# Performance work log

Hardware: AMD Instinct MI355X
Metric: run time of the kernel (lower is better)

The kernel has to match this reference:

```python
import jax, jax.numpy as jnp
import numpy as np

D_MODEL = 1024
D_CODEX = 64
CODEX_SIZE = 8192
BETA = 1.0
EPS_NORM = 1e-12
EPS_LN = 1e-5


def l2norm(x):
    # F.normalize(p=2, dim=-1, eps=1e-12): x / max(||x||, eps)
    n = jnp.sqrt(jnp.sum(x * x, axis=-1, keepdims=True))
    return x / jnp.maximum(n, EPS_NORM)


def setup_inputs() -> dict:
    key = jax.random.key(0)
    ks = jax.random.split(key, 8)
    B, S = 4, 2048
    Z = jax.random.normal(ks[0], (B, S, D_MODEL), dtype=jnp.float32)
    W1 = 0.02 * jax.random.normal(ks[1], (D_MODEL, D_MODEL), dtype=jnp.float32)
    b1 = jnp.zeros((D_MODEL,), dtype=jnp.float32)
    W2 = 0.02 * jax.random.normal(ks[2], (D_MODEL, D_CODEX), dtype=jnp.float32)
    b2 = jnp.zeros((D_CODEX,), dtype=jnp.float32)
    codex = l2norm(jax.random.normal(ks[3], (CODEX_SIZE, D_CODEX), dtype=jnp.float32))
    ln_w = jnp.ones((D_CODEX,), dtype=jnp.float32)
    ln_b = jnp.zeros((D_CODEX,), dtype=jnp.float32)
    Wp = 0.02 * jax.random.normal(ks[4], (D_CODEX, D_MODEL), dtype=jnp.float32)
    bp = jnp.zeros((D_MODEL,), dtype=jnp.float32)
    return {"Z": Z, "W1": W1, "b1": b1, "W2": W2, "b2": b2,
            "codex": codex, "ln_w": ln_w, "ln_b": ln_b, "Wp": Wp, "bp": bp}


def reference(Z, W1, b1, W2, b2, codex, ln_w, ln_b, Wp, bp):
    # pre_proj: Linear -> Tanh -> Linear, then l2-normalize into codex space
    Z_e = jnp.tanh(Z @ W1 + b1) @ W2 + b2            # (B, S, d_codex)
    Z_e = l2norm(Z_e)
    flat = Z_e.reshape(-1, D_CODEX)                  # (N, d_codex)
    # squared-L2 distances: |z|^2 + |c|^2 - 2 z.c
    dists = (jnp.sum(flat * flat, axis=-1, keepdims=True)
             + jnp.sum(codex * codex, axis=-1)[None, :]
             - 2.0 * jnp.einsum('nd,cd->nc', flat, codex))  # (N, K)
    idxs = jnp.argmin(dists, axis=-1).reshape(Z_e.shape[:-1])  # (B, S)
    codex_probs = jax.nn.one_hot(idxs, CODEX_SIZE, dtype=Z_e.dtype)  # (B, S, K)
    Z_q = codex[idxs]                                 # (B, S, d_codex)
    # commitment loss (codex is an EMA buffer, no gradient through it)
    loss = BETA * jnp.mean((jax.lax.stop_gradient(Z_q) - Z_e) ** 2)
    # straight-through estimator
    Z_q = Z_e + jax.lax.stop_gradient(Z_q - Z_e)
    # layernorm over d_codex
    mu = jnp.mean(Z_q, axis=-1, keepdims=True)
    var = jnp.mean((Z_q - mu) ** 2, axis=-1, keepdims=True)
    Z_q = (Z_q - mu) * jax.lax.rsqrt(var + EPS_LN) * ln_w + ln_b
    # post_proj back to d_model
    Z_q = Z_q @ Wp + bp                               # (B, S, d_model)
    return Z_q, loss, codex_probs
```

## Files before the change

kernel.cpp:

```cpp
#include <hip/hip_runtime.h>
#include <math.h>
#include <stdint.h>

#define N_TOK   8192
#define DMODEL  1024
#define DCODEX  64
#define KCODES  8192

typedef short short8 __attribute__((ext_vector_type(8)));
typedef float f32x16 __attribute__((ext_vector_type(16)));

union Frag { short8 s; uint2 u[2]; };

__device__ __forceinline__ unsigned short f2bf(float f) {
    unsigned u = __float_as_uint(f);
    unsigned r = u + 0x7FFFu + ((u >> 16) & 1u);
    return (unsigned short)(r >> 16);
}
__device__ __forceinline__ float bf2f(unsigned short h) {
    return __uint_as_float(((unsigned)h) << 16);
}

__global__ __launch_bounds__(256) void codenorm_kernel(const float* __restrict__ codex,
                                                       float* __restrict__ cn2) {
    int k = blockIdx.x * 256 + threadIdx.x;
    const float4* p = (const float4*)(codex + (size_t)k * DCODEX);
    float s = 0.f;
#pragma unroll
    for (int i = 0; i < 16; ++i) {
        float4 v = p[i];
        s += v.x * v.x + v.y * v.y + v.z * v.z + v.w * v.w;
    }
    cn2[k] = s;
}

__global__ __launch_bounds__(256) void split_w1_kernel(const float* __restrict__ W1,
                                                       unsigned short* __restrict__ t0,
                                                       unsigned short* __restrict__ t1,
                                                       unsigned short* __restrict__ t2) {
    __shared__ float tile[32][33];
    const int tid = threadIdx.x;
    const int k0 = blockIdx.x * 32;
    const int n0 = blockIdx.y * 32;
    {
        int i = tid >> 3, j4 = (tid & 7) * 4;
        float4 v = *(const float4*)(W1 + (size_t)(k0 + i) * DMODEL + n0 + j4);
        tile[i][j4 + 0] = v.x; tile[i][j4 + 1] = v.y;
        tile[i][j4 + 2] = v.z; tile[i][j4 + 3] = v.w;
    }
    __syncthreads();
    int n = tid >> 3, kq = (tid & 7) * 4;
    ushort4 h0, h1, h2;
#pragma unroll
    for (int c = 0; c < 4; ++c) {
        float f = tile[kq + c][n];
        unsigned short a0 = f2bf(f);
        float r1 = f - bf2f(a0);
        unsigned short a1 = f2bf(r1);
        float r2 = r1 - bf2f(a1);
        unsigned short a2 = f2bf(r2);
        ((unsigned short*)&h0)[c] = a0;
        ((unsigned short*)&h1)[c] = a1;
        ((unsigned short*)&h2)[c] = a2;
    }
    size_t off = (size_t)(n0 + n) * DMODEL + k0 + kq;
    *(ushort4*)(t0 + off) = h0;
    *(ushort4*)(t1 + off) = h1;
    *(ushort4*)(t2 + off) = h2;
}

__global__ __launch_bounds__(256) void gemm1_mfma_kernel(const float* __restrict__ Z,
                                                         const unsigned short* __restrict__ W1t0,
                                                         const unsigned short* __restrict__ W1t1,
                                                         const unsigned short* __restrict__ W1t2,
                                                         const float* __restrict__ b1,
                                                         float* __restrict__ H) {
    __shared__ unsigned short Ash[3][128][36];
    __shared__ unsigned short Bsh[3][128][36];
    const int tid = threadIdx.x;
    const int row0 = blockIdx.x * 128;
    const int col0 = blockIdx.y * 128;
    const int wave = tid >> 6;
    const int lane = tid & 63;
    const int lrow = lane & 31;
    const int lhalf = lane >> 5;
    const int wm = wave >> 1, wn = wave & 1;

    f32x16 acc[2][2];
#pragma unroll
    for (int i = 0; i < 2; ++i)
#pragma unroll
        for (int j = 0; j < 2; ++j)
#pragma unroll
            for (int r = 0; r < 16; ++r) acc[i][j][r] = 0.f;

    for (int k0 = 0; k0 < DMODEL; k0 += 32) {
        __syncthreads();
#pragma unroll
        for (int t = 0; t < 4; ++t) {
            int q = tid + t * 256;
            int r = q >> 3, kc = (q & 7) * 4;
            float4 v = *(const float4*)(Z + (size_t)(row0 + r) * DMODEL + k0 + kc);
            float f[4] = {v.x, v.y, v.z, v.w};
            unsigned h0[4], h1[4], h2[4];
#pragma unroll
            for (int c = 0; c < 4; ++c) {
                unsigned short a0 = f2bf(f[c]);
                float r1 = f[c] - bf2f(a0);
                unsigned short a1 = f2bf(r1);
                float r2 = r1 - bf2f(a1);
                unsigned short a2 = f2bf(r2);
                h0[c] = a0; h1[c] = a1; h2[c] = a2;
            }
            uint2 p0 = make_uint2(h0[0] | (h0[1] << 16), h0[2] | (h0[3] << 16));
            uint2 p1 = make_uint2(h1[0] | (h1[1] << 16), h1[2] | (h1[3] << 16));
            uint2 p2 = make_uint2(h2[0] | (h2[1] << 16), h2[2] | (h2[3] << 16));
            *(uint2*)&Ash[0][r][kc] = p0;
            *(uint2*)&Ash[1][r][kc] = p1;
            *(uint2*)&Ash[2][r][kc] = p2;
        }
#pragma unroll
        for (int t = 0; t < 6; ++t) {
            int e = tid + t * 256;
            int l = e >> 9;
            int rem = e & 511;
            int n = rem >> 2, kq = (rem & 3) * 8;
            const unsigned short* src = (l == 0) ? W1t0 : (l == 1) ? W1t1 : W1t2;
            uint4 v = *(const uint4*)(src + (size_t)(col0 + n) * DMODEL + k0 + kq);
            *(uint2*)&Bsh[l][n][kq]     = make_uint2(v.x, v.y);
            *(uint2*)&Bsh[l][n][kq + 4] = make_uint2(v.z, v.w);
        }
        __syncthreads();
#pragma unroll
        for (int mk = 0; mk < 2; ++mk) {
            const int kb = mk * 16 + lhalf * 8;
            Frag ah[2], am[2], al[2], bh[2], bm[2], bl[2];
#pragma unroll
            for (int ti = 0; ti < 2; ++ti) {
                int rA = wm * 64 + ti * 32 + lrow;
                ah[ti].u[0] = *(const uint2*)&Ash[0][rA][kb];
                ah[ti].u[1] = *(const uint2*)&Ash[0][rA][kb + 4];
                am[ti].u[0] = *(const uint2*)&Ash[1][rA][kb];
                am[ti].u[1] = *(const uint2*)&Ash[1][rA][kb + 4];
                al[ti].u[0] = *(const uint2*)&Ash[2][rA][kb];
                al[ti].u[1] = *(const uint2*)&Ash[2][rA][kb + 4];
            }
#pragma unroll
            for (int tj = 0; tj < 2; ++tj) {
                int rB = wn * 64 + tj * 32 + lrow;
                bh[tj].u[0] = *(const uint2*)&Bsh[0][rB][kb];
                bh[tj].u[1] = *(const uint2*)&Bsh[0][rB][kb + 4];
                bm[tj].u[0] = *(const uint2*)&Bsh[1][rB][kb];
                bm[tj].u[1] = *(const uint2*)&Bsh[1][rB][kb + 4];
                bl[tj].u[0] = *(const uint2*)&Bsh[2][rB][kb];
                bl[tj].u[1] = *(const uint2*)&Bsh[2][rB][kb + 4];
            }
#pragma unroll
            for (int ti = 0; ti < 2; ++ti)
#pragma unroll
                for (int tj = 0; tj < 2; ++tj) {
                    acc[ti][tj] = __builtin_amdgcn_mfma_f32_32x32x16_bf16(ah[ti].s, bh[tj].s, acc[ti][tj], 0, 0, 0);
                    acc[ti][tj] = __builtin_amdgcn_mfma_f32_32x32x16_bf16(ah[ti].s, bm[tj].s, acc[ti][tj], 0, 0, 0);
                    acc[ti][tj] = __builtin_amdgcn_mfma_f32_32x32x16_bf16(am[ti].s, bh[tj].s, acc[ti][tj], 0, 0, 0);
                    acc[ti][tj] = __builtin_amdgcn_mfma_f32_32x32x16_bf16(am[ti].s, bm[tj].s, acc[ti][tj], 0, 0, 0);
                    acc[ti][tj] = __builtin_amdgcn_mfma_f32_32x32x16_bf16(ah[ti].s, bl[tj].s, acc[ti][tj], 0, 0, 0);
                    acc[ti][tj] = __builtin_amdgcn_mfma_f32_32x32x16_bf16(al[ti].s, bh[tj].s, acc[ti][tj], 0, 0, 0);
                }
        }
    }

    float b1v[2];
#pragma unroll
    for (int tj = 0; tj < 2; ++tj) b1v[tj] = b1[col0 + wn * 64 + tj * 32 + lrow];
#pragma unroll
    for (int ti = 0; ti < 2; ++ti)
#pragma unroll
        for (int tj = 0; tj < 2; ++tj) {
            int col = col0 + wn * 64 + tj * 32 + lrow;
#pragma unroll
            for (int r = 0; r < 16; ++r) {
                int row = row0 + wm * 64 + ti * 32 + (r & 3) + 8 * (r >> 2) + 4 * lhalf;
                H[(size_t)row * DMODEL + col] = tanhf(acc[ti][tj][r] + b1v[tj]);
            }
        }
}

__global__ __launch_bounds__(256) void gemm2_norm_kernel(const float* __restrict__ H,
                                                         const float* __restrict__ W2,
                                                         const float* __restrict__ b2,
                                                         float* __restrict__ Ze) {
    __shared__ float As[64][36];
    __shared__ float Bs[64][68];
    const int tid = threadIdx.x;
    const int row0 = blockIdx.x * 32;
    const int ty = tid >> 4, tx = tid & 15;

    float acc[2][4];
#pragma unroll
    for (int i = 0; i < 2; ++i)
#pragma unroll
        for (int j = 0; j < 4; ++j) acc[i][j] = 0.f;

    for (int k0 = 0; k0 < DMODEL; k0 += 64) {
        __syncthreads();
#pragma unroll
        for (int t = 0; t < 2; ++t) {
            int q = tid + t * 256;
            int r = q >> 4, k4 = (q & 15) * 4;
            float4 v = *(const float4*)(H + (size_t)(row0 + r) * DMODEL + k0 + k4);
            As[k4 + 0][r] = v.x; As[k4 + 1][r] = v.y;
            As[k4 + 2][r] = v.z; As[k4 + 3][r] = v.w;
        }
#pragma unroll
        for (int t = 0; t < 4; ++t) {
            int q = tid + t * 256;
            int kk = q >> 4, c4 = (q & 15) * 4;
            *(float4*)&Bs[kk][c4] = *(const float4*)(W2 + (size_t)(k0 + kk) * DCODEX + c4);
        }
        __syncthreads();
#pragma unroll
        for (int k = 0; k < 64; ++k) {
            float2 a = *(const float2*)&As[k][ty * 2];
            float4 b = *(const float4*)&Bs[k][tx * 4];
            float bw[4] = {b.x, b.y, b.z, b.w};
#pragma unroll
            for (int j = 0; j < 4; ++j) {
                acc[0][j] = fmaf(a.x, bw[j], acc[0][j]);
                acc[1][j] = fmaf(a.y, bw[j], acc[1][j]);
            }
        }
    }
    float4 b2v4 = *(const float4*)(b2 + tx * 4);
    float b2v[4] = {b2v4.x, b2v4.y, b2v4.z, b2v4.w};
#pragma unroll
    for (int i = 0; i < 2; ++i) {
        float e[4];
#pragma unroll
        for (int j = 0; j < 4; ++j) e[j] = acc[i][j] + b2v[j];
        float ss = e[0] * e[0] + e[1] * e[1] + e[2] * e[2] + e[3] * e[3];
        ss += __shfl_xor(ss, 8, 64);
        ss += __shfl_xor(ss, 4, 64);
        ss += __shfl_xor(ss, 2, 64);
        ss += __shfl_xor(ss, 1, 64);
        float nrm = fmaxf(sqrtf(ss), 1e-12f);
        float o[4];
#pragma unroll
        for (int j = 0; j < 4; ++j) o[j] = e[j] / nrm;
        *(float4*)(Ze + (size_t)(row0 + ty * 2 + i) * DCODEX + tx * 4) = *(float4*)&o[0];
    }
}

__device__ __forceinline__ unsigned fenc(float f) {
    unsigned u = __float_as_uint(f);
    return (u & 0x80000000u) ? ~u : (u | 0x80000000u);
}

__global__ __launch_bounds__(256) void dist_argmin_kernel(const float* __restrict__ Ze,
                                                          const float* __restrict__ codex,
                                                          const float* __restrict__ cn2,
                                                          unsigned long long* __restrict__ gbest) {
    __shared__ float Zs[64][132];
    __shared__ float Cs[32][132];
    __shared__ unsigned long long red[128];
    const int tid = threadIdx.x;
    const int row0 = blockIdx.x * 128;
    const int strip0 = blockIdx.y * 1024;
    const int ty = tid >> 4, tx = tid & 15;

    if (tid < 128) red[tid] = 0xFFFFFFFFFFFFFFFFull;
#pragma unroll
    for (int t = 0; t < 8; ++t) {
        int q = tid + t * 256;
        int r = q >> 4, d4 = (q & 15) * 4;
        float4 v = *(const float4*)(Ze + (size_t)(row0 + r) * DCODEX + d4);
        Zs[d4 + 0][r] = v.x; Zs[d4 + 1][r] = v.y;
        Zs[d4 + 2][r] = v.z; Zs[d4 + 3][r] = v.w;
    }

    float bv[8];
    int bi[8];
#pragma unroll
    for (int i = 0; i < 8; ++i) { bv[i] = INFINITY; bi[i] = 0; }

    for (int c0 = 0; c0 < 1024; c0 += 128) {
        const int cbase = strip0 + c0;
        float cn[8];
        *(float4*)&cn[0] = *(const float4*)(cn2 + cbase + tx * 4);
        *(float4*)&cn[4] = *(const float4*)(cn2 + cbase + 64 + tx * 4);
        float s[8][8];
#pragma unroll
        for (int i = 0; i < 8; ++i)
#pragma unroll
            for (int j = 0; j < 8; ++j) s[i][j] = 0.f;

        for (int h = 0; h < 2; ++h) {
            __syncthreads();
#pragma unroll
            for (int t = 0; t < 4; ++t) {
                int q = tid + t * 256;
                int c = q >> 3, d4 = (q & 7) * 4;
                float4 v = *(const float4*)(codex + (size_t)(cbase + c) * DCODEX + h * 32 + d4);
                Cs[d4 + 0][c] = v.x; Cs[d4 + 1][c] = v.y;
                Cs[d4 + 2][c] = v.z; Cs[d4 + 3][c] = v.w;
            }
            __syncthreads();
#pragma unroll
            for (int d = 0; d < 32; ++d) {
                float a[8], b[8];
                *(float4*)&a[0] = *(const float4*)&Zs[h * 32 + d][ty * 4];
                *(float4*)&a[4] = *(const float4*)&Zs[h * 32 + d][64 + ty * 4];
                *(float4*)&b[0] = *(const float4*)&Cs[d][tx * 4];
                *(float4*)&b[4] = *(const float4*)&Cs[d][64 + tx * 4];
#pragma unroll
                for (int i = 0; i < 8; ++i)
#pragma unroll
                    for (int j = 0; j < 8; ++j)
                        s[i][j] = fmaf(a[i], b[j], s[i][j]);
            }
        }
#pragma unroll
        for (int i = 0; i < 8; ++i)
#pragma unroll
            for (int j = 0; j < 8; ++j) {
                float dist = fmaf(-2.0f, s[i][j], cn[j]);
                int col = cbase + ((j < 4) ? (tx * 4 + j) : (64 + tx * 4 + j - 4));
                if (dist < bv[i]) { bv[i] = dist; bi[i] = col; }
            }
    }
#pragma unroll
    for (int i = 0; i < 8; ++i) {
        int li = (i < 4) ? (ty * 4 + i) : (64 + ty * 4 + i - 4);
        unsigned long long key =
            ((unsigned long long)fenc(bv[i]) << 32) | (unsigned)bi[i];
        atomicMin(&red[li], key);
    }
    __syncthreads();
    if (tid < 128) atomicMin(&gbest[row0 + tid], red[tid]);
}

__global__ __launch_bounds__(256) void zero_scatter_kernel(const unsigned long long* __restrict__ gbest,
                                                           float* __restrict__ probs) {
    size_t g = (size_t)blockIdx.x * 256 + threadIdx.x;
    int row = (int)(g >> 11);
    int c4i = (int)(g & 2047);
    unsigned id = (unsigned)(gbest[row] & 0xFFFFFFFFull);
    float4 v = {0.f, 0.f, 0.f, 0.f};
    if ((id >> 2) == (unsigned)c4i) ((float*)&v)[id & 3] = 1.0f;
    *(float4*)(probs + ((size_t)row << 13) + ((size_t)c4i << 2)) = v;
}

__global__ __launch_bounds__(256) void ln_loss_kernel(const unsigned long long* __restrict__ gbest,
                                                      const float* __restrict__ codex,
                                                      const float* __restrict__ Ze,
                                                      const float* __restrict__ ln_w,
                                                      const float* __restrict__ ln_b,
                                                      float* __restrict__ Aln,
                                                      float* __restrict__ loss) {
    const int tid = threadIdx.x;
    const int w = tid >> 6, l = tid & 63;
    const int row = blockIdx.x * 4 + w;
    int id = (int)(unsigned)(gbest[row] & 0xFFFFFFFFull);
    float zq = codex[(size_t)id * DCODEX + l];
    float ze = Ze[(size_t)row * DCODEX + l];
    float dlt = zq - ze;
    float val = ze + dlt;
    float s = val;
#pragma unroll
    for (int m = 32; m >= 1; m >>= 1) s += __shfl_xor(s, m, 64);
    float mu = s * 0.015625f;
    float c = val - mu;
    float v2 = c * c;
#pragma unroll
    for (int m = 32; m >= 1; m >>= 1) v2 += __shfl_xor(v2, m, 64);
    float var = v2 * 0.015625f;
    float y = c * (1.0f / sqrtf(var + 1e-5f)) * ln_w[l] + ln_b[l];
    Aln[(size_t)row * DCODEX + l] = y;
    float d2 = dlt * dlt;
#pragma unroll
    for (int m = 32; m >= 1; m >>= 1) d2 += __shfl_xor(d2, m, 64);
    if (l == 0) atomicAdd(loss, d2 * (1.0f / 524288.0f));
}

__global__ __launch_bounds__(256) void gemm3_kernel(const float* __restrict__ Aln,
                                                    const float* __restrict__ Wp,
                                                    const float* __restrict__ bp,
                                                    float* __restrict__ Zq) {
    __shared__ float As[64][132];
    __shared__ float Bs[64][68];
    const int tid = threadIdx.x;
    const int row0 = blockIdx.x * 128;
    const int col0 = blockIdx.y * 64;
    const int ty = tid >> 4, tx = tid & 15;

#pragma unroll
    for (int t = 0; t < 8; ++t) {
        int q = tid + t * 256;
        int r = q >> 4, d4 = (q & 15) * 4;
        float4 v = *(const float4*)(Aln + (size_t)(row0 + r) * DCODEX + d4);
        As[d4 + 0][r] = v.x; As[d4 + 1][r] = v.y;
        As[d4 + 2][r] = v.z; As[d4 + 3][r] = v.w;
    }
#pragma unroll
    for (int t = 0; t < 4; ++t) {
        int q = tid + t * 256;
        int kk = q >> 4, c4 = (q & 15) * 4;
        *(float4*)&Bs[kk][c4] = *(const float4*)(Wp + (size_t)kk * DMODEL + col0 + c4);
    }
    __syncthreads();

    float acc[8][4];
#pragma unroll
    for (int i = 0; i < 8; ++i)
#pragma unroll
        for (int j = 0; j < 4; ++j) acc[i][j] = 0.f;
#pragma unroll
    for (int k = 0; k < 64; ++k) {
        float a[8];
        *(float4*)&a[0] = *(const float4*)&As[k][ty * 4];
        *(float4*)&a[4] = *(const float4*)&As[k][64 + ty * 4];
        float4 b = *(const float4*)&Bs[k][tx * 4];
        float bw[4] = {b.x, b.y, b.z, b.w};
#pragma unroll
        for (int i = 0; i < 8; ++i)
#pragma unroll
            for (int j = 0; j < 4; ++j)
                acc[i][j] = fmaf(a[i], bw[j], acc[i][j]);
    }
    float4 bp4 = *(const float4*)(bp + col0 + tx * 4);
    float bb[4] = {bp4.x, bp4.y, bp4.z, bp4.w};
#pragma unroll
    for (int half = 0; half < 2; ++half)
#pragma unroll
        for (int i = 0; i < 4; ++i) {
            int r = row0 + half * 64 + ty * 4 + i;
            float o[4];
#pragma unroll
            for (int j = 0; j < 4; ++j) o[j] = acc[half * 4 + i][j] + bb[j];
            *(float4*)(Zq + (size_t)r * DMODEL + col0 + tx * 4) = *(float4*)&o[0];
        }
}

extern "C" void kernel_launch(void* const* d_in, const int* in_sizes, int n_in,
                              void* d_out, int out_size, void* d_ws, size_t ws_size,
                              hipStream_t stream) {
    const float* Z     = (const float*)d_in[0];
    const float* W1    = (const float*)d_in[1];
    const float* b1    = (const float*)d_in[2];
    const float* W2    = (const float*)d_in[3];
    const float* b2    = (const float*)d_in[4];
    const float* codex = (const float*)d_in[5];
    const float* ln_w  = (const float*)d_in[6];
    const float* ln_b  = (const float*)d_in[7];
    const float* Wp    = (const float*)d_in[8];
    const float* bp    = (const float*)d_in[9];

    float* out      = (float*)d_out;
    float* Zq_out   = out;
    float* loss_out = out + (size_t)N_TOK * DMODEL;
    float* probs    = loss_out + 1;

    char* ws = (char*)d_ws;
    float* H   = (float*)ws;
    float* Aln = H;
    float* Ze  = H + (size_t)N_TOK * DMODEL;
    float* cn2 = Ze + (size_t)N_TOK * DCODEX;
    unsigned long long* gbest = (unsigned long long*)(cn2 + KCODES);
    unsigned short* W1t0 = (unsigned short*)(gbest + N_TOK);
    unsigned short* W1t1 = W1t0 + (size_t)DMODEL * DMODEL;
    unsigned short* W1t2 = W1t1 + (size_t)DMODEL * DMODEL;

    hipMemsetAsync(loss_out, 0, sizeof(float), stream);
    hipMemsetAsync(gbest, 0xFF, (size_t)N_TOK * sizeof(unsigned long long), stream);

    codenorm_kernel<<<KCODES / 256, 256, 0, stream>>>(codex, cn2);
    split_w1_kernel<<<dim3(DMODEL / 32, DMODEL / 32), 256, 0, stream>>>(W1, W1t0, W1t1, W1t2);
    gemm1_mfma_kernel<<<dim3(N_TOK / 128, DMODEL / 128), 256, 0, stream>>>(Z, W1t0, W1t1, W1t2, b1, H);
    gemm2_norm_kernel<<<N_TOK / 32, 256, 0, stream>>>(H, W2, b2, Ze);
    dist_argmin_kernel<<<dim3(N_TOK / 128, KCODES / 1024), 256, 0, stream>>>(Ze, codex, cn2, gbest);
    zero_scatter_kernel<<<(int)(((size_t)N_TOK * KCODES / 4) / 256), 256, 0, stream>>>(gbest, probs);
    ln_loss_kernel<<<N_TOK / 4, 256, 0, stream>>>(gbest, codex, Ze, ln_w, ln_b, Aln, loss_out);
    gemm3_kernel<<<dim3(N_TOK / 128, DMODEL / 64), 256, 0, stream>>>(Aln, Wp, bp, Zq_out);
}
```

Baseline: 731.5 us.

## Move distance GEMM to split-bf16 MFMA and pre-split Z outside gemm1

Replaces the FP32 FMA distance/argmin kernel with an MFMA kernel that uses a three-way bf16 split (six products per tile) on pre-split Ze and codex arrays, reducing argmin with wave shuffles and a 64-bit atomicMin. It also pre-splits Z into three bf16 planes in a separate pass so gemm1 only loads bf16 tiles instead of splitting inside every block. The cost is extra split kernels, more workspace, extra global traffic for the Z planes, and more blocks doing atomics on gbest. Split-bf16 accuracy could also flip argmin ties in rare cases.

```diff
diff --git a/kernel.cpp b/kernel.cpp
--- a/kernel.cpp
+++ b/kernel.cpp
@@ -32,6 +32,30 @@
         s += v.x * v.x + v.y * v.y + v.z * v.z + v.w * v.w;
     }
     cn2[k] = s;
+}
+
+__global__ __launch_bounds__(256) void split3_kernel(const float* __restrict__ src,
+                                                     unsigned short* __restrict__ p0,
+                                                     unsigned short* __restrict__ p1,
+                                                     unsigned short* __restrict__ p2) {
+    size_t i4 = ((size_t)blockIdx.x * 256 + threadIdx.x) * 4;
+    float4 v = *(const float4*)(src + i4);
+    float f[4] = {v.x, v.y, v.z, v.w};
+    ushort4 h0, h1, h2;
+#pragma unroll
+    for (int c = 0; c < 4; ++c) {
+        unsigned short a0 = f2bf(f[c]);
+        float r1 = f[c] - bf2f(a0);
+        unsigned short a1 = f2bf(r1);
+        float r2 = r1 - bf2f(a1);
+        unsigned short a2 = f2bf(r2);
+        ((unsigned short*)&h0)[c] = a0;
+        ((unsigned short*)&h1)[c] = a1;
+        ((unsigned short*)&h2)[c] = a2;
+    }
+    *(ushort4*)(p0 + i4) = h0;
+    *(ushort4*)(p1 + i4) = h1;
+    *(ushort4*)(p2 + i4) = h2;
 }
 
 __global__ __launch_bounds__(256) void split_w1_kernel(const float* __restrict__ W1,
@@ -69,7 +93,9 @@
     *(ushort4*)(t2 + off) = h2;
 }
 
-__global__ __launch_bounds__(256) void gemm1_mfma_kernel(const float* __restrict__ Z,
+__global__ __launch_bounds__(256) void gemm1_mfma_kernel(const unsigned short* __restrict__ Zt0,
+                                                         const unsigned short* __restrict__ Zt1,
+                                                         const unsigned short* __restrict__ Zt2,
                                                          const unsigned short* __restrict__ W1t0,
                                                          const unsigned short* __restrict__ W1t1,
                                                          const unsigned short* __restrict__ W1t2,
@@ -86,6 +112,9 @@
     const int lhalf = lane >> 5;
     const int wm = wave >> 1, wn = wave & 1;
 
+    const unsigned short* Ap[3] = {Zt0, Zt1, Zt2};
+    const unsigned short* Bp[3] = {W1t0, W1t1, W1t2};
+
     f32x16 acc[2][2];
 #pragma unroll
     for (int i = 0; i < 2; ++i)
@@ -97,38 +126,18 @@
     for (int k0 = 0; k0 < DMODEL; k0 += 32) {
         __syncthreads();
 #pragma unroll
-        for (int t = 0; t < 4; ++t) {
-            int q = tid + t * 256;
-            int r = q >> 3, kc = (q & 7) * 4;
-            float4 v = *(const float4*)(Z + (size_t)(row0 + r) * DMODEL + k0 + kc);
-            float f[4] = {v.x, v.y, v.z, v.w};
-            unsigned h0[4], h1[4], h2[4];
-#pragma unroll
-            for (int c = 0; c < 4; ++c) {
-                unsigned short a0 = f2bf(f[c]);
-                float r1 = f[c] - bf2f(a0);
-                unsigned short a1 = f2bf(r1);
-                float r2 = r1 - bf2f(a1);
-                unsigned short a2 = f2bf(r2);
-                h0[c] = a0; h1[c] = a1; h2[c] = a2;
-            }
-            uint2 p0 = make_uint2(h0[0] | (h0[1] << 16), h0[2] | (h0[3] << 16));
-            uint2 p1 = make_uint2(h1[0] | (h1[1] << 16), h1[2] | (h1[3] << 16));
-            uint2 p2 = make_uint2(h2[0] | (h2[1] << 16), h2[2] | (h2[3] << 16));
-            *(uint2*)&Ash[0][r][kc] = p0;
-            *(uint2*)&Ash[1][r][kc] = p1;
-            *(uint2*)&Ash[2][r][kc] = p2;
-        }
-#pragma unroll
-        for (int t = 0; t < 6; ++t) {
-            int e = tid + t * 256;
-            int l = e >> 9;
-            int rem = e & 511;
-            int n = rem >> 2, kq = (rem & 3) * 8;
-            const unsigned short* src = (l == 0) ? W1t0 : (l == 1) ? W1t1 : W1t2;
-            uint4 v = *(const uint4*)(src + (size_t)(col0 + n) * DMODEL + k0 + kq);
-            *(uint2*)&Bsh[l][n][kq]     = make_uint2(v.x, v.y);
-            *(uint2*)&Bsh[l][n][kq + 4] = make_uint2(v.z, v.w);
+        for (int l = 0; l < 3; ++l) {
+#pragma unroll
+            for (int t = 0; t < 2; ++t) {
+                int q = tid + t * 256;
+                int r = q >> 2, kq = (q & 3) * 8;
+                uint4 va = *(const uint4*)(Ap[l] + (size_t)(row0 + r) * DMODEL + k0 + kq);
+                *(uint2*)&Ash[l][r][kq]     = make_uint2(va.x, va.y);
+                *(uint2*)&Ash[l][r][kq + 4] = make_uint2(va.z, va.w);
+                uint4 vb = *(const uint4*)(Bp[l] + (size_t)(col0 + r) * DMODEL + k0 + kq);
+                *(uint2*)&Bsh[l][r][kq]     = make_uint2(vb.x, vb.y);
+                *(uint2*)&Bsh[l][r][kq + 4] = make_uint2(vb.z, vb.w);
+            }
         }
         __syncthreads();
 #pragma unroll
@@ -254,85 +263,121 @@
     unsigned u = __float_as_uint(f);
     return (u & 0x80000000u) ? ~u : (u | 0x80000000u);
 }
-
-__global__ __launch_bounds__(256) void dist_argmin_kernel(const float* __restrict__ Ze,
-                                                          const float* __restrict__ codex,
-                                                          const float* __restrict__ cn2,
-                                                          unsigned long long* __restrict__ gbest) {
-    __shared__ float Zs[64][132];
-    __shared__ float Cs[32][132];
+__device__ __forceinline__ unsigned long long ullmin2(unsigned long long a,
+                                                      unsigned long long b) {
+    return a < b ? a : b;
+}
+
+__global__ __launch_bounds__(256) void dist_mfma_kernel(const unsigned short* __restrict__ Zh,
+                                                        const unsigned short* __restrict__ Zm,
+                                                        const unsigned short* __restrict__ Zl,
+                                                        const unsigned short* __restrict__ Ch,
+                                                        const unsigned short* __restrict__ Cm,
+                                                        const unsigned short* __restrict__ Cl,
+                                                        const float* __restrict__ cn2,
+                                                        unsigned long long* __restrict__ gbest) {
+    __shared__ unsigned short Ash[3][128][36];
+    __shared__ unsigned short Bsh[3][128][36];
     __shared__ unsigned long long red[128];
     const int tid = threadIdx.x;
     const int row0 = blockIdx.x * 128;
-    const int strip0 = blockIdx.y * 1024;
-    const int ty = tid >> 4, tx = tid & 15;
+    const int col0 = blockIdx.y * 128;
+    const int wave = tid >> 6;
+    const int lane = tid & 63;
+    const int lrow = lane & 31;
+    const int lhalf = lane >> 5;
+    const int wm = wave >> 1, wn = wave & 1;
+
+    const unsigned short* Ap[3] = {Zh, Zm, Zl};
+    const unsigned short* Bp[3] = {Ch, Cm, Cl};
 
     if (tid < 128) red[tid] = 0xFFFFFFFFFFFFFFFFull;
-#pragma unroll
-    for (int t = 0; t < 8; ++t) {
-        int q = tid + t * 256;
-        int r = q >> 4, d4 = (q & 15) * 4;
-        float4 v = *(const float4*)(Ze + (size_t)(row0 + r) * DCODEX + d4);
-        Zs[d4 + 0][r] = v.x; Zs[d4 + 1][r] = v.y;
-        Zs[d4 + 2][r] = v.z; Zs[d4 + 3][r] = v.w;
-    }
-
-    float bv[8];
-    int bi[8];
-#pragma unroll
-    for (int i = 0; i < 8; ++i) { bv[i] = INFINITY; bi[i] = 0; }
-
-    for (int c0 = 0; c0 < 1024; c0 += 128) {
-        const int cbase = strip0 + c0;
-        float cn[8];
-        *(float4*)&cn[0] = *(const float4*)(cn2 + cbase + tx * 4);
-        *(float4*)&cn[4] = *(const float4*)(cn2 + cbase + 64 + tx * 4);
-        float s[8][8];
-#pragma unroll
-        for (int i = 0; i < 8; ++i)
-#pragma unroll
-            for (int j = 0; j < 8; ++j) s[i][j] = 0.f;
-
-        for (int h = 0; h < 2; ++h) {
-            __syncthreads();
-#pragma unroll
-            for (int t = 0; t < 4; ++t) {
+
+    f32x16 acc[2][2];
+#pragma unroll
+    for (int i = 0; i < 2; ++i)
+#pragma unroll
+        for (int j = 0; j < 2; ++j)
+#pragma unroll
+            for (int r = 0; r < 16; ++r) acc[i][j][r] = 0.f;
+
+#pragma unroll
+    for (int k0 = 0; k0 < DCODEX; k0 += 32) {
+        __syncthreads();
+#pragma unroll
+        for (int l = 0; l < 3; ++l) {
+#pragma unroll
+            for (int t = 0; t < 2; ++t) {
                 int q = tid + t * 256;
-                int c = q >> 3, d4 = (q & 7) * 4;
-                float4 v = *(const float4*)(codex + (size_t)(cbase + c) * DCODEX + h * 32 + d4);
-                Cs[d4 + 0][c] = v.x; Cs[d4 + 1][c] = v.y;
-                Cs[d4 + 2][c] = v.z; Cs[d4 + 3][c] = v.w;
-            }
-            __syncthreads();
-#pragma unroll
-            for (int d = 0; d < 32; ++d) {
-                float a[8], b[8];
-                *(float4*)&a[0] = *(const float4*)&Zs[h * 32 + d][ty * 4];
-                *(float4*)&a[4] = *(const float4*)&Zs[h * 32 + d][64 + ty * 4];
-                *(float4*)&b[0] = *(const float4*)&Cs[d][tx * 4];
-                *(float4*)&b[4] = *(const float4*)&Cs[d][64 + tx * 4];
-#pragma unroll
-                for (int i = 0; i < 8; ++i)
-#pragma unroll
-                    for (int j = 0; j < 8; ++j)
-                        s[i][j] = fmaf(a[i], b[j], s[i][j]);
-            }
-        }
-#pragma unroll
-        for (int i = 0; i < 8; ++i)
-#pragma unroll
-            for (int j = 0; j < 8; ++j) {
-                float dist = fmaf(-2.0f, s[i][j], cn[j]);
-                int col = cbase + ((j < 4) ? (tx * 4 + j) : (64 + tx * 4 + j - 4));
-                if (dist < bv[i]) { bv[i] = dist; bi[i] = col; }
-            }
-    }
-#pragma unroll
-    for (int i = 0; i < 8; ++i) {
-        int li = (i < 4) ? (ty * 4 + i) : (64 + ty * 4 + i - 4);
-        unsigned long long key =
-            ((unsigned long long)fenc(bv[i]) << 32) | (unsigned)bi[i];
-        atomicMin(&red[li], key);
+                int r = q >> 2, kq = (q & 3) * 8;
+                uint4 va = *(const uint4*)(Ap[l] + (size_t)(row0 + r) * DCODEX + k0 + kq);
+                *(uint2*)&Ash[l][r][kq]     = make_uint2(va.x, va.y);
+                *(uint2*)&Ash[l][r][kq + 4] = make_uint2(va.z, va.w);
+                uint4 vb = *(const uint4*)(Bp[l] + (size_t)(col0 + r) * DCODEX + k0 + kq);
+                *(uint2*)&Bsh[l][r][kq]     = make_uint2(vb.x, vb.y);
+                *(uint2*)&Bsh[l][r][kq + 4] = make_uint2(vb.z, vb.w);
+            }
+        }
+        __syncthreads();
+#pragma unroll
+        for (int mk = 0; mk < 2; ++mk) {
+            const int kb = mk * 16 + lhalf * 8;
+            Frag ah[2], am[2], al[2], bh[2], bm[2], bl[2];
+#pragma unroll
+            for (int ti = 0; ti < 2; ++ti) {
+                int rA = wm * 64 + ti * 32 + lrow;
+                ah[ti].u[0] = *(const uint2*)&Ash[0][rA][kb];
+                ah[ti].u[1] = *(const uint2*)&Ash[0][rA][kb + 4];
+                am[ti].u[0] = *(const uint2*)&Ash[1][rA][kb];
+                am[ti].u[1] = *(const uint2*)&Ash[1][rA][kb + 4];
+                al[ti].u[0] = *(const uint2*)&Ash[2][rA][kb];
+                al[ti].u[1] = *(const uint2*)&Ash[2][rA][kb + 4];
+            }
+#pragma unroll
+            for (int tj = 0; tj < 2; ++tj) {
+                int rB = wn * 64 + tj * 32 + lrow;
+                bh[tj].u[0] = *(const uint2*)&Bsh[0][rB][kb];
+                bh[tj].u[1] = *(const uint2*)&Bsh[0][rB][kb + 4];
+                bm[tj].u[0] = *(const uint2*)&Bsh[1][rB][kb];
+                bm[tj].u[1] = *(const uint2*)&Bsh[1][rB][kb + 4];
+                bl[tj].u[0] = *(const uint2*)&Bsh[2][rB][kb];
+                bl[tj].u[1] = *(const uint2*)&Bsh[2][rB][kb + 4];
+            }
+#pragma unroll
+            for (int ti = 0; ti < 2; ++ti)
+#pragma unroll
+                for (int tj = 0; tj < 2; ++tj) {
+                    acc[ti][tj] = __builtin_amdgcn_mfma_f32_32x32x16_bf16(ah[ti].s, bh[tj].s, acc[ti][tj], 0, 0, 0);
+                    acc[ti][tj] = __builtin_amdgcn_mfma_f32_32x32x16_bf16(ah[ti].s, bm[tj].s, acc[ti][tj], 0, 0, 0);
+                    acc[ti][tj] = __builtin_amdgcn_mfma_f32_32x32x16_bf16(am[ti].s, bh[tj].s, acc[ti][tj], 0, 0, 0);
+                    acc[ti][tj] = __builtin_amdgcn_mfma_f32_32x32x16_bf16(am[ti].s, bm[tj].s, acc[ti][tj], 0, 0, 0);
+                    acc[ti][tj] = __builtin_amdgcn_mfma_f32_32x32x16_bf16(ah[ti].s, bl[tj].s, acc[ti][tj], 0, 0, 0);
+                    acc[ti][tj] = __builtin_amdgcn_mfma_f32_32x32x16_bf16(al[ti].s, bh[tj].s, acc[ti][tj], 0, 0, 0);
+                }
+        }
+    }
+
+    float cnv[2];
+#pragma unroll
+    for (int tj = 0; tj < 2; ++tj) cnv[tj] = cn2[col0 + wn * 64 + tj * 32 + lrow];
+#pragma unroll
+    for (int ti = 0; ti < 2; ++ti) {
+#pragma unroll
+        for (int r = 0; r < 16; ++r) {
+            int rloc = wm * 64 + ti * 32 + (r & 3) + 8 * (r >> 2) + 4 * lhalf;
+            unsigned long long kmin = 0xFFFFFFFFFFFFFFFFull;
+#pragma unroll
+            for (int tj = 0; tj < 2; ++tj) {
+                float dist = fmaf(-2.0f, acc[ti][tj][r], cnv[tj]);
+                unsigned col = (unsigned)(col0 + wn * 64 + tj * 32 + lrow);
+                unsigned long long key = ((unsigned long long)fenc(dist) << 32) | col;
+                kmin = ullmin2(kmin, key);
+            }
+#pragma unroll
+            for (int m = 1; m <= 16; m <<= 1)
+                kmin = ullmin2(kmin, (unsigned long long)__shfl_xor((long long)kmin, m, 64));
+            if (lrow == 0) atomicMin(&red[rloc], kmin);
+        }
     }
     __syncthreads();
     if (tid < 128) atomicMin(&gbest[row0 + tid], red[tid]);
@@ -468,15 +513,27 @@
     unsigned short* W1t0 = (unsigned short*)(gbest + N_TOK);
     unsigned short* W1t1 = W1t0 + (size_t)DMODEL * DMODEL;
     unsigned short* W1t2 = W1t1 + (size_t)DMODEL * DMODEL;
+    unsigned short* Zt0  = W1t2 + (size_t)DMODEL * DMODEL;
+    unsigned short* Zt1  = Zt0 + (size_t)N_TOK * DMODEL;
+    unsigned short* Zt2  = Zt1 + (size_t)N_TOK * DMODEL;
+    unsigned short* Zeh  = Zt2 + (size_t)N_TOK * DMODEL;
+    unsigned short* Zem  = Zeh + (size_t)N_TOK * DCODEX;
+    unsigned short* Zel  = Zem + (size_t)N_TOK * DCODEX;
+    unsigned short* Chh  = Zel + (size_t)N_TOK * DCODEX;
+    unsigned short* Chm  = Chh + (size_t)KCODES * DCODEX;
+    unsigned short* Chl  = Chm + (size_t)KCODES * DCODEX;
 
     hipMemsetAsync(loss_out, 0, sizeof(float), stream);
     hipMemsetAsync(gbest, 0xFF, (size_t)N_TOK * sizeof(unsigned long long), stream);
 
     codenorm_kernel<<<KCODES / 256, 256, 0, stream>>>(codex, cn2);
     split_w1_kernel<<<dim3(DMODEL / 32, DMODEL / 32), 256, 0, stream>>>(W1, W1t0, W1t1, W1t2);
-    gemm1_mfma_kernel<<<dim3(N_TOK / 128, DMODEL / 128), 256, 0, stream>>>(Z, W1t0, W1t1, W1t2, b1, H);
+    split3_kernel<<<(int)(((size_t)N_TOK * DMODEL) / 1024), 256, 0, stream>>>(Z, Zt0, Zt1, Zt2);
+    split3_kernel<<<(int)(((size_t)KCODES * DCODEX) / 1024), 256, 0, stream>>>(codex, Chh, Chm, Chl);
+    gemm1_mfma_kernel<<<dim3(N_TOK / 128, DMODEL / 128), 256, 0, stream>>>(Zt0, Zt1, Zt2, W1t0, W1t1, W1t2, b1, H);
     gemm2_norm_kernel<<<N_TOK / 32, 256, 0, stream>>>(H, W2, b2, Ze);
-    dist_argmin_kernel<<<dim3(N_TOK / 128, KCODES / 1024), 256, 0, stream>>>(Ze, codex, cn2, gbest);
+    split3_kernel<<<(int)(((size_t)N_TOK * DCODEX) / 1024), 256, 0, stream>>>(Ze, Zeh, Zem, Zel);
+    dist_mfma_kernel<<<dim3(N_TOK / 128, KCODES / 128), 256, 0, stream>>>(Zeh, Zem, Zel, Chh, Chm, Chl, cn2, gbest);
     zero_scatter_kernel<<<(int)(((size_t)N_TOK * KCODES / 4) / 256), 256, 0, stream>>>(gbest, probs);
     ln_loss_kernel<<<N_TOK / 4, 256, 0, stream>>>(gbest, codex, Ze, ln_w, ln_b, Aln, loss_out);
     gemm3_kernel<<<dim3(N_TOK / 128, DMODEL / 64), 256, 0, stream>>>(Aln, Wp, bp, Zq_out);
```

New measurement: 773.4 us. +5.7%, slower.
